# Optimization experiments

Measured on AMD Instinct MI355X. Metric: run time of the kernel, lower is better.

## Reference

```python
import jax, jax.numpy as jnp
import numpy as np

B, MAX_NODE, MEM_LEN, DIM, HEADS, LAYERS, DEG = 32, 1024, 256, 128, 4, 4, 16
CH = DIM // HEADS


def setup_inputs() -> dict:
    key = jax.random.key(0)
    ks = jax.random.split(key, 16)
    counts = np.array([512 + 16 * i for i in range(B)])  # ragged graph sizes, sum = 24320
    N = int(counts.sum())
    node2batch = np.repeat(np.arange(B), counts)
    node2pos = np.concatenate([np.arange(c) for c in counts])
    bmask = np.arange(MAX_NODE)[None, :] < counts[:, None]
    rng = np.random.default_rng(0)
    srcs, dsts, off = [], [], 0
    for c in counts:  # edges stay within each graph
        srcs.append(off + rng.integers(0, c, size=DEG * c))
        dsts.append(off + rng.integers(0, c, size=DEG * c))
        off += c
    edge_index = np.stack([np.concatenate(srcs), np.concatenate(dsts)])

    def rn(k, shape, scale=0.05):
        return jax.random.normal(k, shape, jnp.float32) * scale

    return dict(
        node_feats=rn(ks[0], (N, DIM), 1.0),
        edge_feats=rn(ks[1], (edge_index.shape[1], DIM), 1.0),
        memory=rn(ks[2], (B, MEM_LEN, DIM), 1.0),
        Wn=rn(ks[3], (LAYERS, DIM, DIM)), bn=jnp.zeros((LAYERS, DIM)),
        We=rn(ks[4], (LAYERS, DIM, DIM)),
        att_src=rn(ks[5], (LAYERS, HEADS, CH)),
        att_dst=rn(ks[6], (LAYERS, HEADS, CH)),
        att_edge=rn(ks[7], (LAYERS, HEADS, CH)),
        ln1_g=jnp.ones((LAYERS, DIM)), ln1_b=jnp.zeros((LAYERS, DIM)),
        ln2_g=jnp.ones((LAYERS, DIM)), ln2_b=jnp.zeros((LAYERS, DIM)),
        Wq=rn(ks[8], (LAYERS, DIM, DIM)), Wk=rn(ks[9], (LAYERS, DIM, DIM)),
        Wv=rn(ks[10], (LAYERS, DIM, DIM)), Wo=rn(ks[11], (LAYERS, DIM, DIM)),
        Ew1=rn(ks[12], (LAYERS, 3 * DIM, DIM)), Eb1=jnp.zeros((LAYERS, DIM)),
        Ew2=rn(ks[13], (LAYERS, DIM, DIM)), Eb2=jnp.zeros((LAYERS, DIM)),
        edge_index=jnp.asarray(edge_index, jnp.int32),
        node2batch=jnp.asarray(node2batch, jnp.int32),
        node2pos=jnp.asarray(node2pos, jnp.int32),
        batch_mask=jnp.asarray(bmask),
        mem_pad_mask=jnp.ones((B, MEM_LEN), bool),
    )


def _ln(x, g, b):
    mu = x.mean(-1, keepdims=True)
    v = ((x - mu) ** 2).mean(-1, keepdims=True)
    return (x - mu) * jax.lax.rsqrt(v + 1e-5) * g + b


def reference(node_feats, edge_feats, memory, Wn, bn, We, att_src, att_dst, att_edge,
              ln1_g, ln1_b, ln2_g, ln2_b, Wq, Wk, Wv, Wo, Ew1, Eb1, Ew2, Eb2,
              edge_index, node2batch, node2pos, batch_mask, mem_pad_mask):
    N = node_feats.shape[0]
    src, dst = edge_index[0], edge_index[1]
    # [B, max_node, mem_len]: attend only valid memory slots from valid nodes
    cross_mask = mem_pad_mask[:, None, :] & batch_mask[:, :, None]
    x, e = node_feats, edge_feats
    for l in range(LAYERS):
        # --- edge-conditioned GAT conv (segment softmax over dst) ---
        h = (x @ Wn[l]).reshape(N, HEADS, CH)
        eh = (e @ We[l]).reshape(-1, HEADS, CH)
        logits = (h[src] * att_src[l]).sum(-1) + (h[dst] * att_dst[l]).sum(-1) + (eh * att_edge[l]).sum(-1)
        logits = jax.nn.leaky_relu(logits, 0.2)  # [E, H]
        m = jax.ops.segment_max(logits, dst, num_segments=N)
        ew = jnp.exp(logits - m[dst])
        den = jax.ops.segment_sum(ew, dst, num_segments=N)
        alpha = ew / (den[dst] + 1e-16)
        conv = jax.ops.segment_sum(alpha[..., None] * (h[src] + eh), dst, num_segments=N)
        conv = conv.reshape(N, DIM) + bn[l]
        x = jax.nn.relu(_ln(conv, ln1_g[l], ln1_b[l])) + x
        # --- graph2batch scatter into dense padded tensor ---
        dense = jnp.zeros((B, MAX_NODE, DIM), x.dtype).at[node2batch, node2pos].set(x)
        # --- cross attention against memory ---
        q = (dense @ Wq[l]).reshape(B, MAX_NODE, HEADS, CH)
        k = (memory @ Wk[l]).reshape(B, MEM_LEN, HEADS, CH)
        v = (memory @ Wv[l]).reshape(B, MEM_LEN, HEADS, CH)
        scores = jnp.einsum('bqhc,bkhc->bhqk', q, k) / np.float32(np.sqrt(CH))
        scores = jnp.where(cross_mask[:, None], scores, jnp.float32(-1e9))
        ao = jnp.einsum('bhqk,bkhc->bqhc', jax.nn.softmax(scores, axis=-1), v)
        ao = ao.reshape(B, MAX_NODE, DIM) @ Wo[l]
        dense = jax.nn.relu(_ln(ao + dense, ln2_g[l], ln2_b[l]))
        x = dense[node2batch, node2pos]  # batch2graph gather
        # --- residual sparse edge update ---
        ecat = jnp.concatenate([e, x[src], x[dst]], axis=-1)
        e = e + jax.nn.relu(ecat @ Ew1[l] + Eb1[l]) @ Ew2[l] + Eb2[l]
    return x, e
```

## Files before the change

kernel.cpp:

```cpp
#include <hip/hip_runtime.h>

#define DIM    128
#define HEADS  4
#define CH     32
#define MEMLEN 256
#define LAYERS 4


__global__ void copy_f4(const float4* __restrict__ in, float4* __restrict__ out, long n) {
    long i = (long)blockIdx.x * blockDim.x + threadIdx.x;
    long stride = (long)gridDim.x * blockDim.x;
    for (; i < n; i += stride) out[i] = in[i];
}

__global__ void hist_k(const int* __restrict__ dst, int E, int* __restrict__ deg) {
    int e = blockIdx.x * blockDim.x + threadIdx.x;
    if (e < E) atomicAdd(&deg[dst[e]], 1);
}

__global__ void csr_offsets(const int* __restrict__ deg, int n, int* __restrict__ off) {
    __shared__ int part[1024];
    int t = threadIdx.x;
    int chunk = (n + 1023) >> 10;
    int lo = t * chunk, hi = min(lo + chunk, n);
    int s = 0;
    for (int i = lo; i < hi; i++) s += deg[i];
    part[t] = s; __syncthreads();
    for (int d = 1; d < 1024; d <<= 1) {
        int v = part[t];
        int add = (t >= d) ? part[t - d] : 0;
        __syncthreads();
        part[t] = v + add;
        __syncthreads();
    }
    int run = (t == 0) ? 0 : part[t - 1];
    for (int i = lo; i < hi; i++) { off[i] = run; run += deg[i]; }
    if (t == 1023) off[n] = part[1023];
}

__global__ void csr_fill(const int* __restrict__ dst, int E, const int* __restrict__ off,
                         int* __restrict__ cur, int* __restrict__ csr) {
    int e = blockIdx.x * blockDim.x + threadIdx.x;
    if (e < E) {
        int d = dst[e];
        int p = atomicAdd(&cur[d], 1);
        csr[off[d] + p] = e;
    }
}

__device__ __forceinline__ float block_reduce_sum128(float v, float* red) {
    int t = threadIdx.x;
    red[t] = v; __syncthreads();
#pragma unroll
    for (int s = 64; s > 0; s >>= 1) {
        if (t < s) red[t] += red[t + s];
        __syncthreads();
    }
    float r = red[0]; __syncthreads();
    return r;
}

__global__ __launch_bounds__(256) void gemm128(const float* __restrict__ A,
                                               const float* __restrict__ W,
                                               const float* __restrict__ bias,
                                               float* __restrict__ out, int R) {
    int r0 = blockIdx.x * 64, t = threadIdx.x;
    __shared__ float at[64][DIM];
    for (int i = t; i < 64 * 32; i += 256) {
        int rr = i >> 5, cc = i & 31;
        if (r0 + rr < R)
            ((float4*)at[rr])[cc] = ((const float4*)(A + (size_t)(r0 + rr) * DIM))[cc];
    }
    __syncthreads();
    int c0 = (t & 31) * 4;
    int rb = (t >> 5) * 8;
    float acc[8][4];
#pragma unroll
    for (int ee = 0; ee < 8; ee++)
        acc[ee][0] = acc[ee][1] = acc[ee][2] = acc[ee][3] = 0.f;
    for (int k = 0; k < DIM; k += 4) {
        float4 w0 = *(const float4*)&W[(k + 0) * DIM + c0];
        float4 w1 = *(const float4*)&W[(k + 1) * DIM + c0];
        float4 w2 = *(const float4*)&W[(k + 2) * DIM + c0];
        float4 w3 = *(const float4*)&W[(k + 3) * DIM + c0];
#pragma unroll
        for (int ee = 0; ee < 8; ee++) {
            float4 a = *(float4*)&at[rb + ee][k];
            acc[ee][0] += a.x * w0.x + a.y * w1.x + a.z * w2.x + a.w * w3.x;
            acc[ee][1] += a.x * w0.y + a.y * w1.y + a.z * w2.y + a.w * w3.y;
            acc[ee][2] += a.x * w0.z + a.y * w1.z + a.z * w2.z + a.w * w3.z;
            acc[ee][3] += a.x * w0.w + a.y * w1.w + a.z * w2.w + a.w * w3.w;
        }
    }
    float4 bb = make_float4(0.f, 0.f, 0.f, 0.f);
    if (bias) bb = *(const float4*)&bias[c0];
#pragma unroll
    for (int ee = 0; ee < 8; ee++) {
        int r = r0 + rb + ee;
        if (r < R) {
            float4 o = make_float4(acc[ee][0] + bb.x, acc[ee][1] + bb.y,
                                   acc[ee][2] + bb.z, acc[ee][3] + bb.w);
            *(float4*)&out[(size_t)r * DIM + c0] = o;
        }
    }
}

__global__ __launch_bounds__(256) void node_proj_tile(
    const float* __restrict__ x, const float* __restrict__ W,
    const float* __restrict__ att_s, const float* __restrict__ att_d,
    float* __restrict__ h, float* __restrict__ ssrc, float* __restrict__ sdst, int N) {
    int r0 = blockIdx.x * 64, t = threadIdx.x;
    __shared__ float at[64][DIM];
    for (int i = t; i < 64 * 32; i += 256) {
        int rr = i >> 5, cc = i & 31;
        if (r0 + rr < N)
            ((float4*)at[rr])[cc] = ((const float4*)(x + (size_t)(r0 + rr) * DIM))[cc];
    }
    __syncthreads();
    int c0 = (t & 31) * 4;
    int rb = (t >> 5) * 8;
    float acc[8][4];
#pragma unroll
    for (int ee = 0; ee < 8; ee++)
        acc[ee][0] = acc[ee][1] = acc[ee][2] = acc[ee][3] = 0.f;
    for (int k = 0; k < DIM; k += 4) {
        float4 w0 = *(const float4*)&W[(k + 0) * DIM + c0];
        float4 w1 = *(const float4*)&W[(k + 1) * DIM + c0];
        float4 w2 = *(const float4*)&W[(k + 2) * DIM + c0];
        float4 w3 = *(const float4*)&W[(k + 3) * DIM + c0];
#pragma unroll
        for (int ee = 0; ee < 8; ee++) {
            float4 a = *(float4*)&at[rb + ee][k];
            acc[ee][0] += a.x * w0.x + a.y * w1.x + a.z * w2.x + a.w * w3.x;
            acc[ee][1] += a.x * w0.y + a.y * w1.y + a.z * w2.y + a.w * w3.y;
            acc[ee][2] += a.x * w0.z + a.y * w1.z + a.z * w2.z + a.w * w3.z;
            acc[ee][3] += a.x * w0.w + a.y * w1.w + a.z * w2.w + a.w * w3.w;
        }
    }
    int hh = (t & 31) >> 3;
    float4 as = *(const float4*)&att_s[c0];
    float4 ad = *(const float4*)&att_d[c0];
#pragma unroll
    for (int ee = 0; ee < 8; ee++) {
        int r = r0 + rb + ee;
        if (r < N) {
            *(float4*)&h[(size_t)r * DIM + c0] =
                make_float4(acc[ee][0], acc[ee][1], acc[ee][2], acc[ee][3]);
            float ps = acc[ee][0]*as.x + acc[ee][1]*as.y + acc[ee][2]*as.z + acc[ee][3]*as.w;
            float pd = acc[ee][0]*ad.x + acc[ee][1]*ad.y + acc[ee][2]*ad.z + acc[ee][3]*ad.w;
#pragma unroll
            for (int mk = 1; mk < 8; mk <<= 1) {
                ps += __shfl_xor(ps, mk, 32);
                pd += __shfl_xor(pd, mk, 32);
            }
            if (((t & 31) & 7) == 0) {
                ssrc[r * HEADS + hh] = ps;
                sdst[r * HEADS + hh] = pd;
            }
        }
    }
}


__global__ void make_waE(const float* __restrict__ We, const float* __restrict__ att_e,
                         float* __restrict__ waE) {
    int k = threadIdx.x;
#pragma unroll
    for (int h = 0; h < HEADS; h++) {
        float s = 0.f;
#pragma unroll
        for (int c = 0; c < CH; c++) s += We[k * DIM + h * CH + c] * att_e[h * CH + c];
        waE[k * HEADS + h] = s;
    }
}

__global__ void sedge_logits(const float* __restrict__ e, const float* __restrict__ waE,
                             const float* __restrict__ ssrc, const float* __restrict__ sdst,
                             const int* __restrict__ src, const int* __restrict__ dst,
                             float* __restrict__ lw, int E) {
    __shared__ float w[DIM * HEADS];
    int t = threadIdx.x;
    w[t] = waE[t]; w[t + 256] = waE[t + 256];
    __syncthreads();
    int g = t >> 5, lane = t & 31;
    int eid = blockIdx.x * 8 + g;
    if (eid >= E) return;
    const float* er = e + (size_t)eid * DIM;
    float s0 = 0.f, s1 = 0.f, s2 = 0.f, s3 = 0.f;
#pragma unroll
    for (int j = 0; j < 4; j++) {
        int k = lane + 32 * j;
        float v = er[k];
        s0 += v * w[k * 4 + 0]; s1 += v * w[k * 4 + 1];
        s2 += v * w[k * 4 + 2]; s3 += v * w[k * 4 + 3];
    }
#pragma unroll
    for (int m = 16; m; m >>= 1) {
        s0 += __shfl_xor(s0, m, 32); s1 += __shfl_xor(s1, m, 32);
        s2 += __shfl_xor(s2, m, 32); s3 += __shfl_xor(s3, m, 32);
    }
    if (lane == 0) {
        int sn = src[eid] * HEADS, dn = dst[eid] * HEADS;
        float l0 = ssrc[sn + 0] + sdst[dn + 0] + s0;
        float l1 = ssrc[sn + 1] + sdst[dn + 1] + s1;
        float l2 = ssrc[sn + 2] + sdst[dn + 2] + s2;
        float l3 = ssrc[sn + 3] + sdst[dn + 3] + s3;
        lw[eid * 4 + 0] = (l0 >= 0.f) ? l0 : 0.2f * l0;
        lw[eid * 4 + 1] = (l1 >= 0.f) ? l1 : 0.2f * l1;
        lw[eid * 4 + 2] = (l2 >= 0.f) ? l2 : 0.2f * l2;
        lw[eid * 4 + 3] = (l3 >= 0.f) ? l3 : 0.2f * l3;
    }
}

__global__ void seg_softmax(const int* __restrict__ off, const int* __restrict__ csr,
                            float* __restrict__ lw, float* __restrict__ den, int NH) {
    int i = blockIdx.x * blockDim.x + threadIdx.x;
    if (i >= NH) return;
    int n = i >> 2, hh = i & 3;
    int o0 = off[n], o1 = off[n + 1];
    float m = -1e30f;
    for (int o = o0; o < o1; o++) m = fmaxf(m, lw[csr[o] * HEADS + hh]);
    float s = 0.f;
    for (int o = o0; o < o1; o++) {
        int idx = csr[o] * HEADS + hh;
        float w = __expf(lw[idx] - m);
        lw[idx] = w;
        s += w;
    }
    den[i] = s;
}

__global__ void conv_ln(const int* __restrict__ off, const int* __restrict__ csr,
                        const int* __restrict__ src,
                        const float* __restrict__ lw, const float* __restrict__ den,
                        const float* __restrict__ hbuf, const float* __restrict__ e,
                        const float* __restrict__ We,
                        const float* __restrict__ bn, const float* __restrict__ g,
                        const float* __restrict__ b, float* __restrict__ x, int N) {
    int n = blockIdx.x, t = threadIdx.x, hh = t >> 5;
    __shared__ float agge[HEADS][DIM];
    __shared__ float red[DIM];
    int o0 = off[n], o1 = off[n + 1];
    float acch = 0.f, a0 = 0.f, a1 = 0.f, a2 = 0.f, a3 = 0.f;
    for (int o = o0; o < o1; o++) {
        int eid = csr[o];
        int s = src[eid];
        float4 al = *(const float4*)&lw[eid * 4];
        acch += ((&al.x)[hh]) * hbuf[(size_t)s * DIM + t];
        float ev = e[(size_t)eid * DIM + t];
        a0 += al.x * ev; a1 += al.y * ev; a2 += al.z * ev; a3 += al.w * ev;
    }
    agge[0][t] = a0; agge[1][t] = a1; agge[2][t] = a2; agge[3][t] = a3;
    __syncthreads();
    float ehc = 0.f;
#pragma unroll 8
    for (int k = 0; k < DIM; k++) ehc += agge[hh][k] * We[k * DIM + t];
    float d = den[n * HEADS + hh];
    float conv = (acch + ehc) / (d + 1e-16f) + bn[t];
    float mu = block_reduce_sum128(conv, red) * (1.f / DIM);
    float diff = conv - mu;
    float var = block_reduce_sum128(diff * diff, red) * (1.f / DIM);
    float y = diff * rsqrtf(var + 1e-5f) * g[t] + b[t];
    x[(size_t)n * DIM + t] = fmaxf(y, 0.f) + x[(size_t)n * DIM + t];
}

__global__ void kv_proj(const float* __restrict__ mem, const float* __restrict__ Wk,
                        const float* __restrict__ Wv, float* __restrict__ kb,
                        float* __restrict__ vb, int R) {
    int r = blockIdx.x, t = threadIdx.x;
    __shared__ float row[DIM];
    row[t] = mem[(size_t)r * DIM + t];
    __syncthreads();
    float ak = 0.f, av = 0.f;
#pragma unroll 4
    for (int k = 0; k < DIM; k++) {
        float rv = row[k];
        ak += rv * Wk[k * DIM + t];
        av += rv * Wv[k * DIM + t];
    }
    kb[(size_t)r * DIM + t] = ak;
    vb[(size_t)r * DIM + t] = av;
}

__global__ __launch_bounds__(256) void cross_attn_tile(
    float* __restrict__ x, const float* __restrict__ qg,
    const float* __restrict__ kb, const float* __restrict__ vb,
    const float* __restrict__ Wo, const float* __restrict__ g,
    const float* __restrict__ b, const int* __restrict__ boff) {
    int bb = blockIdx.y;
    int n0 = boff[bb] + blockIdx.x * 64;
    int cnt = boff[bb + 1] - n0;
    if (cnt <= 0) return;
    int nq = min(64, cnt);
    int t = threadIdx.x;
    int q = t & 63, h = t >> 6;

    __shared__ float smem[64 * 132];

    float qv[32];
    if (q < nq) {
        const float4* qp = (const float4*)(qg + (size_t)(n0 + q) * DIM + h * CH);
#pragma unroll
        for (int j = 0; j < 8; j++) {
            float4 v = qp[j];
            qv[4*j+0] = v.x; qv[4*j+1] = v.y; qv[4*j+2] = v.z; qv[4*j+3] = v.w;
        }
    } else {
#pragma unroll
        for (int c = 0; c < 32; c++) qv[c] = 0.f;
    }

    float oacc[32];
#pragma unroll
    for (int c = 0; c < 32; c++) oacc[c] = 0.f;
    float m = -1e30f, l = 0.f;

    const float4* Ksrc = (const float4*)(kb + (size_t)bb * MEMLEN * DIM);
    const float4* Vsrc = (const float4*)(vb + (size_t)bb * MEMLEN * DIM);
    float4* Kl = (float4*)smem;
    float4* Vl = (float4*)(smem + 32 * DIM);

    for (int ch = 0; ch < MEMLEN / 32; ch++) {
        __syncthreads();
#pragma unroll
        for (int r = 0; r < 4; r++) {
            int idx = t + r * 256;
            Kl[idx] = Ksrc[ch * 1024 + idx];
            Vl[idx] = Vsrc[ch * 1024 + idx];
        }
        __syncthreads();
        float sc[32];
#pragma unroll
        for (int kk = 0; kk < 32; kk++) {
            const float* kp = smem + kk * DIM + h * CH;
            float s = 0.f;
#pragma unroll
            for (int c = 0; c < 32; c++) s += qv[c] * kp[c];
            sc[kk] = s * 0.17677669529663689f;
        }
        float mc = sc[0];
#pragma unroll
        for (int kk = 1; kk < 32; kk++) mc = fmaxf(mc, sc[kk]);
        float mn = fmaxf(m, mc);
        float scale = __expf(m - mn);
        m = mn;
        float ls = 0.f;
#pragma unroll
        for (int kk = 0; kk < 32; kk++) {
            float w = __expf(sc[kk] - mn);
            sc[kk] = w;
            ls += w;
        }
        l = l * scale + ls;
#pragma unroll
        for (int c = 0; c < 32; c++) oacc[c] *= scale;
#pragma unroll
        for (int kk = 0; kk < 32; kk++) {
            const float* vp = smem + 32 * DIM + kk * DIM + h * CH;
            float w = sc[kk];
#pragma unroll
            for (int c = 0; c < 32; c++) oacc[c] += w * vp[c];
        }
    }
    __syncthreads();
    {
        float inv = 1.f / l;
        float* ap = smem + q * 132 + h * CH;
#pragma unroll
        for (int c = 0; c < 32; c++) ap[c] = oacc[c] * inv;
    }
    __syncthreads();
    int c0 = (t & 31) * 4;
    int rb = (t >> 5) * 8;
    float acc2[8][4];
#pragma unroll
    for (int ee = 0; ee < 8; ee++)
        acc2[ee][0] = acc2[ee][1] = acc2[ee][2] = acc2[ee][3] = 0.f;
    for (int k = 0; k < DIM; k += 4) {
        float4 w0 = *(const float4*)&Wo[(k + 0) * DIM + c0];
        float4 w1 = *(const float4*)&Wo[(k + 1) * DIM + c0];
        float4 w2 = *(const float4*)&Wo[(k + 2) * DIM + c0];
        float4 w3 = *(const float4*)&Wo[(k + 3) * DIM + c0];
#pragma unroll
        for (int ee = 0; ee < 8; ee++) {
            float4 a = *(const float4*)(smem + (rb + ee) * 132 + k);
            acc2[ee][0] += a.x * w0.x + a.y * w1.x + a.z * w2.x + a.w * w3.x;
            acc2[ee][1] += a.x * w0.y + a.y * w1.y + a.z * w2.y + a.w * w3.y;
            acc2[ee][2] += a.x * w0.z + a.y * w1.z + a.z * w2.z + a.w * w3.z;
            acc2[ee][3] += a.x * w0.w + a.y * w1.w + a.z * w2.w + a.w * w3.w;
        }
    }
    float4 gg = *(const float4*)&g[c0];
    float4 bb4 = *(const float4*)&b[c0];
#pragma unroll
    for (int ee = 0; ee < 8; ee++) {
        int r = rb + ee;
        if (r < nq) {
            float4 xr = *(const float4*)&x[(size_t)(n0 + r) * DIM + c0];
            float o0 = acc2[ee][0] + xr.x, o1 = acc2[ee][1] + xr.y;
            float o2 = acc2[ee][2] + xr.z, o3 = acc2[ee][3] + xr.w;
            float s1 = o0 + o1 + o2 + o3;
#pragma unroll
            for (int mk = 16; mk; mk >>= 1) s1 += __shfl_xor(s1, mk, 32);
            float mu = s1 * (1.f / DIM);
            float d0 = o0 - mu, d1 = o1 - mu, d2 = o2 - mu, d3 = o3 - mu;
            float s2 = d0*d0 + d1*d1 + d2*d2 + d3*d3;
#pragma unroll
            for (int mk = 16; mk; mk >>= 1) s2 += __shfl_xor(s2, mk, 32);
            float rs = rsqrtf(s2 * (1.f / DIM) + 1e-5f);
            float4 o = make_float4(fmaxf(d0 * rs * gg.x + bb4.x, 0.f),
                                   fmaxf(d1 * rs * gg.y + bb4.y, 0.f),
                                   fmaxf(d2 * rs * gg.z + bb4.z, 0.f),
                                   fmaxf(d3 * rs * gg.w + bb4.w, 0.f));
            *(float4*)&x[(size_t)(n0 + r) * DIM + c0] = o;
        }
    }
}

__global__ __launch_bounds__(256) void edge_mlp(float* __restrict__ e,
                                                const float* __restrict__ xs,
                                                const float* __restrict__ xd,
                                                const int* __restrict__ src,
                                                const int* __restrict__ dst,
                                                const float* __restrict__ W1,
                                                const float* __restrict__ W2,
                                                const float* __restrict__ Eb2, int E) {
    int e0 = blockIdx.x * 64, t = threadIdx.x;
    __shared__ float at[64][DIM];
    for (int i = t; i < 64 * 32; i += 256) {
        int rr = i >> 5, cc = i & 31;
        if (e0 + rr < E)
            ((float4*)at[rr])[cc] = ((const float4*)(e + (size_t)(e0 + rr) * DIM))[cc];
    }
    __syncthreads();
    int c0 = (t & 31) * 4;
    int rb = (t >> 5) * 8;
    float acc[8][4];
#pragma unroll
    for (int ee = 0; ee < 8; ee++)
        acc[ee][0] = acc[ee][1] = acc[ee][2] = acc[ee][3] = 0.f;
    for (int k = 0; k < DIM; k += 4) {
        float4 w0 = *(const float4*)&W1[(k + 0) * DIM + c0];
        float4 w1 = *(const float4*)&W1[(k + 1) * DIM + c0];
        float4 w2 = *(const float4*)&W1[(k + 2) * DIM + c0];
        float4 w3 = *(const float4*)&W1[(k + 3) * DIM + c0];
#pragma unroll
        for (int ee = 0; ee < 8; ee++) {
            float4 a = *(float4*)&at[rb + ee][k];
            acc[ee][0] += a.x * w0.x + a.y * w1.x + a.z * w2.x + a.w * w3.x;
            acc[ee][1] += a.x * w0.y + a.y * w1.y + a.z * w2.y + a.w * w3.y;
            acc[ee][2] += a.x * w0.z + a.y * w1.z + a.z * w2.z + a.w * w3.z;
            acc[ee][3] += a.x * w0.w + a.y * w1.w + a.z * w2.w + a.w * w3.w;
        }
    }
#pragma unroll
    for (int ee = 0; ee < 8; ee++) {
        int r = e0 + rb + ee;
        if (r < E) {
            float4 s4 = *(const float4*)&xs[(size_t)src[r] * DIM + c0];
            float4 d4 = *(const float4*)&xd[(size_t)dst[r] * DIM + c0];
            acc[ee][0] = fmaxf(acc[ee][0] + s4.x + d4.x, 0.f);
            acc[ee][1] = fmaxf(acc[ee][1] + s4.y + d4.y, 0.f);
            acc[ee][2] = fmaxf(acc[ee][2] + s4.z + d4.z, 0.f);
            acc[ee][3] = fmaxf(acc[ee][3] + s4.w + d4.w, 0.f);
        }
    }
    __syncthreads();
#pragma unroll
    for (int ee = 0; ee < 8; ee++)
        *(float4*)&at[rb + ee][c0] = make_float4(acc[ee][0], acc[ee][1], acc[ee][2], acc[ee][3]);
    __syncthreads();
#pragma unroll
    for (int ee = 0; ee < 8; ee++)
        acc[ee][0] = acc[ee][1] = acc[ee][2] = acc[ee][3] = 0.f;
    for (int k = 0; k < DIM; k += 4) {
        float4 w0 = *(const float4*)&W2[(k + 0) * DIM + c0];
        float4 w1 = *(const float4*)&W2[(k + 1) * DIM + c0];
        float4 w2 = *(const float4*)&W2[(k + 2) * DIM + c0];
        float4 w3 = *(const float4*)&W2[(k + 3) * DIM + c0];
#pragma unroll
        for (int ee = 0; ee < 8; ee++) {
            float4 a = *(float4*)&at[rb + ee][k];
            acc[ee][0] += a.x * w0.x + a.y * w1.x + a.z * w2.x + a.w * w3.x;
            acc[ee][1] += a.x * w0.y + a.y * w1.y + a.z * w2.y + a.w * w3.y;
            acc[ee][2] += a.x * w0.z + a.y * w1.z + a.z * w2.z + a.w * w3.z;
            acc[ee][3] += a.x * w0.w + a.y * w1.w + a.z * w2.w + a.w * w3.w;
        }
    }
    float4 b2 = *(const float4*)&Eb2[c0];
#pragma unroll
    for (int ee = 0; ee < 8; ee++) {
        int r = e0 + rb + ee;
        if (r < E) {
            float4 old = *(const float4*)&e[(size_t)r * DIM + c0];
            float4 o = make_float4(old.x + acc[ee][0] + b2.x, old.y + acc[ee][1] + b2.y,
                                   old.z + acc[ee][2] + b2.z, old.w + acc[ee][3] + b2.w);
            *(float4*)&e[(size_t)r * DIM + c0] = o;
        }
    }
}


extern "C" void kernel_launch(void* const* d_in, const int* in_sizes, int n_in,
                              void* d_out, int out_size, void* d_ws, size_t ws_size,
                              hipStream_t stream) {
    const float* node_feats = (const float*)d_in[0];
    const float* edge_feats = (const float*)d_in[1];
    const float* memory     = (const float*)d_in[2];
    const float* Wn   = (const float*)d_in[3];
    const float* bn   = (const float*)d_in[4];
    const float* We   = (const float*)d_in[5];
    const float* att_src  = (const float*)d_in[6];
    const float* att_dst  = (const float*)d_in[7];
    const float* att_edge = (const float*)d_in[8];
    const float* ln1_g = (const float*)d_in[9];
    const float* ln1_b = (const float*)d_in[10];
    const float* ln2_g = (const float*)d_in[11];
    const float* ln2_b = (const float*)d_in[12];
    const float* Wq = (const float*)d_in[13];
    const float* Wk = (const float*)d_in[14];
    const float* Wv = (const float*)d_in[15];
    const float* Wo = (const float*)d_in[16];
    const float* Ew1 = (const float*)d_in[17];
    const float* Eb1 = (const float*)d_in[18];
    const float* Ew2 = (const float*)d_in[19];
    const float* Eb2 = (const float*)d_in[20];
    const int* edge_index = (const int*)d_in[21];
    const int* node2batch = (const int*)d_in[22];

    const int N = in_sizes[0] / DIM;
    const int E = in_sizes[1] / DIM;
    const int Bn = in_sizes[2] / (MEMLEN * DIM);
    const int* srcA = edge_index;
    const int* dstA = edge_index + E;

    float* x = (float*)d_out;
    float* e = x + (size_t)N * DIM;

    char* p = (char*)d_ws;
    auto carve = [&](size_t bytes) {
        void* r = (void*)p;
        p += (bytes + 255) & ~(size_t)255;
        return r;
    };
    float* h     = (float*)carve((size_t)N * DIM * 4);
    float* qg    = (float*)carve((size_t)N * DIM * 4);
    float* xs    = (float*)carve((size_t)N * DIM * 4);
    float* xd    = (float*)carve((size_t)N * DIM * 4);
    float* ssrc  = (float*)carve((size_t)N * HEADS * 4);
    float* sdst  = (float*)carve((size_t)N * HEADS * 4);
    float* lw    = (float*)carve((size_t)E * HEADS * 4);
    float* den   = (float*)carve((size_t)N * HEADS * 4);
    float* waE   = (float*)carve((size_t)DIM * HEADS * 4);
    float* kbuf  = (float*)carve((size_t)Bn * MEMLEN * DIM * 4);
    float* vbuf  = (float*)carve((size_t)Bn * MEMLEN * DIM * 4);
    int* deg     = (int*)carve((size_t)N * 4);
    int* cur     = (int*)carve((size_t)N * 4);
    int* off     = (int*)carve(((size_t)N + 1) * 4);
    int* csr     = (int*)carve((size_t)E * 4);
    int* bcnt    = (int*)carve((size_t)Bn * 4);
    int* boff    = (int*)carve(((size_t)Bn + 1) * 4);

    {
        long nx = (long)N * DIM / 4;
        copy_f4<<<dim3(2048), dim3(256), 0, stream>>>((const float4*)node_feats, (float4*)x, nx);
        long nen = (long)E * DIM / 4;
        copy_f4<<<dim3(4096), dim3(256), 0, stream>>>((const float4*)edge_feats, (float4*)e, nen);
    }

    hipMemsetAsync(deg, 0, (size_t)N * 4, stream);
    hipMemsetAsync(cur, 0, (size_t)N * 4, stream);
    hipMemsetAsync(bcnt, 0, (size_t)Bn * 4, stream);
    hist_k<<<dim3((E + 255) / 256), dim3(256), 0, stream>>>(dstA, E, deg);
    csr_offsets<<<dim3(1), dim3(1024), 0, stream>>>(deg, N, off);
    csr_fill<<<dim3((E + 255) / 256), dim3(256), 0, stream>>>(dstA, E, off, cur, csr);
    hist_k<<<dim3((N + 255) / 256), dim3(256), 0, stream>>>(node2batch, N, bcnt);
    csr_offsets<<<dim3(1), dim3(1024), 0, stream>>>(bcnt, Bn, boff);

    const int mrows = Bn * MEMLEN;
    const int maxTiles = 1024 / 64;
    for (int l = 0; l < LAYERS; l++) {
        const float* Wn_l  = Wn  + (size_t)l * DIM * DIM;
        const float* We_l  = We  + (size_t)l * DIM * DIM;
        const float* Wq_l  = Wq  + (size_t)l * DIM * DIM;
        const float* Wk_l  = Wk  + (size_t)l * DIM * DIM;
        const float* Wv_l  = Wv  + (size_t)l * DIM * DIM;
        const float* Wo_l  = Wo  + (size_t)l * DIM * DIM;
        const float* Ew1_l = Ew1 + (size_t)l * 3 * DIM * DIM;
        const float* Ew2_l = Ew2 + (size_t)l * DIM * DIM;

        node_proj_tile<<<dim3((N + 63) / 64), dim3(256), 0, stream>>>(
            x, Wn_l, att_src + l * DIM, att_dst + l * DIM, h, ssrc, sdst, N);
        make_waE<<<dim3(1), dim3(DIM), 0, stream>>>(We_l, att_edge + l * DIM, waE);
        sedge_logits<<<dim3((E + 7) / 8), dim3(256), 0, stream>>>(
            e, waE, ssrc, sdst, srcA, dstA, lw, E);
        seg_softmax<<<dim3((N * HEADS + 255) / 256), dim3(256), 0, stream>>>(
            off, csr, lw, den, N * HEADS);
        conv_ln<<<dim3(N), dim3(DIM), 0, stream>>>(
            off, csr, srcA, lw, den, h, e, We_l,
            bn + l * DIM, ln1_g + l * DIM, ln1_b + l * DIM, x, N);
        kv_proj<<<dim3(mrows), dim3(DIM), 0, stream>>>(
            memory, Wk_l, Wv_l, kbuf, vbuf, mrows);
        gemm128<<<dim3((N + 63) / 64), dim3(256), 0, stream>>>(
            x, Wq_l, nullptr, qg, N);
        cross_attn_tile<<<dim3(maxTiles, Bn), dim3(256), 0, stream>>>(
            x, qg, kbuf, vbuf, Wo_l, ln2_g + l * DIM, ln2_b + l * DIM, boff);
        gemm128<<<dim3((N + 63) / 64), dim3(256), 0, stream>>>(
            x, Ew1_l + (size_t)DIM * DIM, Eb1 + l * DIM, xs, N);
        gemm128<<<dim3((N + 63) / 64), dim3(256), 0, stream>>>(
            x, Ew1_l + (size_t)2 * DIM * DIM, nullptr, xd, N);
        edge_mlp<<<dim3((E + 63) / 64), dim3(256), 0, stream>>>(
            e, xs, xd, srcA, dstA, Ew1_l, Ew2_l, Eb2 + l * DIM, E);
    }
}
```

Baseline: 4.300 ms.

## Split conv aggregation across four edge partitions, retile edge MLP, use gemm for KV

Replaces the per-node 128-thread conv_ln with a 512-thread variant that divides each node's incoming edges over four partitions, reduces the partial sums in shared memory, and uses wave shuffles for the layernorm reductions. The edge MLP is retiled to 4 rows by 8 columns per thread with padded shared rows. The per-row kv_proj kernel is replaced by two calls to the tiled gemm128. The aim is more parallelism per node and better register reuse in the edge GEMMs, at the cost of extra shared-memory reductions and one more launch.

Measured after the change: 4.336 ms. Within noise of the previous version (+0.8%).

```diff
diff --git a/kernel.cpp b/kernel.cpp
--- a/kernel.cpp
+++ b/kernel.cpp
@@ -48,18 +48,6 @@
     }
 }
 
-__device__ __forceinline__ float block_reduce_sum128(float v, float* red) {
-    int t = threadIdx.x;
-    red[t] = v; __syncthreads();
-#pragma unroll
-    for (int s = 64; s > 0; s >>= 1) {
-        if (t < s) red[t] += red[t + s];
-        __syncthreads();
-    }
-    float r = red[0]; __syncthreads();
-    return r;
-}
-
 __global__ __launch_bounds__(256) void gemm128(const float* __restrict__ A,
                                                const float* __restrict__ W,
                                                const float* __restrict__ bias,
@@ -230,56 +218,63 @@
     den[i] = s;
 }
 
-__global__ void conv_ln(const int* __restrict__ off, const int* __restrict__ csr,
-                        const int* __restrict__ src,
-                        const float* __restrict__ lw, const float* __restrict__ den,
-                        const float* __restrict__ hbuf, const float* __restrict__ e,
-                        const float* __restrict__ We,
-                        const float* __restrict__ bn, const float* __restrict__ g,
-                        const float* __restrict__ b, float* __restrict__ x, int N) {
-    int n = blockIdx.x, t = threadIdx.x, hh = t >> 5;
-    __shared__ float agge[HEADS][DIM];
-    __shared__ float red[DIM];
+__global__ __launch_bounds__(512) void conv_ln4(
+    const int* __restrict__ off, const int* __restrict__ csr, const int* __restrict__ src,
+    const float* __restrict__ lw, const float* __restrict__ den,
+    const float* __restrict__ hbuf, const float* __restrict__ e, const float* __restrict__ We,
+    const float* __restrict__ bn, const float* __restrict__ g, const float* __restrict__ b,
+    float* __restrict__ x, int N) {
+    int t = threadIdx.x;
+    int tt = t & 127, part = t >> 7;
+    int n = blockIdx.x;
+    int hh = tt >> 5;
+    __shared__ float aggeP[4][HEADS][DIM];
+    __shared__ float acchP[4][DIM];
+    __shared__ float ehcP[4][DIM];
+    __shared__ float wred[16];
     int o0 = off[n], o1 = off[n + 1];
     float acch = 0.f, a0 = 0.f, a1 = 0.f, a2 = 0.f, a3 = 0.f;
-    for (int o = o0; o < o1; o++) {
+    for (int o = o0 + part; o < o1; o += 4) {
         int eid = csr[o];
         int s = src[eid];
         float4 al = *(const float4*)&lw[eid * 4];
-        acch += ((&al.x)[hh]) * hbuf[(size_t)s * DIM + t];
-        float ev = e[(size_t)eid * DIM + t];
+        acch += ((&al.x)[hh]) * hbuf[(size_t)s * DIM + tt];
+        float ev = e[(size_t)eid * DIM + tt];
         a0 += al.x * ev; a1 += al.y * ev; a2 += al.z * ev; a3 += al.w * ev;
     }
-    agge[0][t] = a0; agge[1][t] = a1; agge[2][t] = a2; agge[3][t] = a3;
+    aggeP[part][0][tt] = a0; aggeP[part][1][tt] = a1;
+    aggeP[part][2][tt] = a2; aggeP[part][3][tt] = a3;
+    acchP[part][tt] = acch;
     __syncthreads();
     float ehc = 0.f;
-#pragma unroll 8
-    for (int k = 0; k < DIM; k++) ehc += agge[hh][k] * We[k * DIM + t];
-    float d = den[n * HEADS + hh];
-    float conv = (acch + ehc) / (d + 1e-16f) + bn[t];
-    float mu = block_reduce_sum128(conv, red) * (1.f / DIM);
+    int k0 = part * 32;
+    for (int k = k0; k < k0 + 32; k++) {
+        float ag = aggeP[0][hh][k] + aggeP[1][hh][k] + aggeP[2][hh][k] + aggeP[3][hh][k];
+        ehc += ag * We[k * DIM + tt];
+    }
+    ehcP[part][tt] = ehc;
+    __syncthreads();
+    float conv = (acchP[0][tt] + acchP[1][tt] + acchP[2][tt] + acchP[3][tt]
+                + ehcP[0][tt] + ehcP[1][tt] + ehcP[2][tt] + ehcP[3][tt])
+                 / (den[n * HEADS + hh] + 1e-16f) + bn[tt];
+    int w = t >> 6;
+    float s1 = conv;
+#pragma unroll
+    for (int mk = 32; mk; mk >>= 1) s1 += __shfl_xor(s1, mk, 64);
+    if ((t & 63) == 0) wred[w] = s1;
+    __syncthreads();
+    float mu = (wred[w] + wred[w ^ 1]) * (1.f / DIM);
     float diff = conv - mu;
-    float var = block_reduce_sum128(diff * diff, red) * (1.f / DIM);
-    float y = diff * rsqrtf(var + 1e-5f) * g[t] + b[t];
-    x[(size_t)n * DIM + t] = fmaxf(y, 0.f) + x[(size_t)n * DIM + t];
-}
-
-__global__ void kv_proj(const float* __restrict__ mem, const float* __restrict__ Wk,
-                        const float* __restrict__ Wv, float* __restrict__ kb,
-                        float* __restrict__ vb, int R) {
-    int r = blockIdx.x, t = threadIdx.x;
-    __shared__ float row[DIM];
-    row[t] = mem[(size_t)r * DIM + t];
-    __syncthreads();
-    float ak = 0.f, av = 0.f;
-#pragma unroll 4
-    for (int k = 0; k < DIM; k++) {
-        float rv = row[k];
-        ak += rv * Wk[k * DIM + t];
-        av += rv * Wv[k * DIM + t];
-    }
-    kb[(size_t)r * DIM + t] = ak;
-    vb[(size_t)r * DIM + t] = av;
+    float s2 = diff * diff;
+#pragma unroll
+    for (int mk = 32; mk; mk >>= 1) s2 += __shfl_xor(s2, mk, 64);
+    if ((t & 63) == 0) wred[8 + w] = s2;
+    __syncthreads();
+    float var = (wred[8 + w] + wred[8 + (w ^ 1)]) * (1.f / DIM);
+    if (part == 0) {
+        float y = diff * rsqrtf(var + 1e-5f) * g[tt] + b[tt];
+        x[(size_t)n * DIM + tt] = fmaxf(y, 0.f) + x[(size_t)n * DIM + tt];
+    }
 }
 
 __global__ __launch_bounds__(256) void cross_attn_tile(
@@ -417,85 +412,119 @@
     }
 }
 
-__global__ __launch_bounds__(256) void edge_mlp(float* __restrict__ e,
-                                                const float* __restrict__ xs,
-                                                const float* __restrict__ xd,
-                                                const int* __restrict__ src,
-                                                const int* __restrict__ dst,
-                                                const float* __restrict__ W1,
-                                                const float* __restrict__ W2,
-                                                const float* __restrict__ Eb2, int E) {
+__global__ __launch_bounds__(256, 4) void edge_mlp(float* __restrict__ e,
+                                                   const float* __restrict__ xs,
+                                                   const float* __restrict__ xd,
+                                                   const int* __restrict__ src,
+                                                   const int* __restrict__ dst,
+                                                   const float* __restrict__ W1,
+                                                   const float* __restrict__ W2,
+                                                   const float* __restrict__ Eb2, int E) {
     int e0 = blockIdx.x * 64, t = threadIdx.x;
-    __shared__ float at[64][DIM];
+    int tx = t & 15, ty = t >> 4;
+    int c0 = tx * 8;
+    __shared__ float at[64][130];
     for (int i = t; i < 64 * 32; i += 256) {
         int rr = i >> 5, cc = i & 31;
         if (e0 + rr < E)
-            ((float4*)at[rr])[cc] = ((const float4*)(e + (size_t)(e0 + rr) * DIM))[cc];
-    }
-    __syncthreads();
-    int c0 = (t & 31) * 4;
-    int rb = (t >> 5) * 8;
-    float acc[8][4];
-#pragma unroll
-    for (int ee = 0; ee < 8; ee++)
-        acc[ee][0] = acc[ee][1] = acc[ee][2] = acc[ee][3] = 0.f;
+            *(float4*)&at[rr][cc * 4] = *(const float4*)&e[(size_t)(e0 + rr) * DIM + cc * 4];
+    }
+    __syncthreads();
+    float acc[4][8];
+#pragma unroll
+    for (int r = 0; r < 4; r++)
+#pragma unroll
+        for (int c = 0; c < 8; c++) acc[r][c] = 0.f;
     for (int k = 0; k < DIM; k += 4) {
-        float4 w0 = *(const float4*)&W1[(k + 0) * DIM + c0];
-        float4 w1 = *(const float4*)&W1[(k + 1) * DIM + c0];
-        float4 w2 = *(const float4*)&W1[(k + 2) * DIM + c0];
-        float4 w3 = *(const float4*)&W1[(k + 3) * DIM + c0];
-#pragma unroll
-        for (int ee = 0; ee < 8; ee++) {
-            float4 a = *(float4*)&at[rb + ee][k];
-            acc[ee][0] += a.x * w0.x + a.y * w1.x + a.z * w2.x + a.w * w3.x;
-            acc[ee][1] += a.x * w0.y + a.y * w1.y + a.z * w2.y + a.w * w3.y;
-            acc[ee][2] += a.x * w0.z + a.y * w1.z + a.z * w2.z + a.w * w3.z;
-            acc[ee][3] += a.x * w0.w + a.y * w1.w + a.z * w2.w + a.w * w3.w;
-        }
-    }
-#pragma unroll
-    for (int ee = 0; ee < 8; ee++) {
-        int r = e0 + rb + ee;
-        if (r < E) {
-            float4 s4 = *(const float4*)&xs[(size_t)src[r] * DIM + c0];
-            float4 d4 = *(const float4*)&xd[(size_t)dst[r] * DIM + c0];
-            acc[ee][0] = fmaxf(acc[ee][0] + s4.x + d4.x, 0.f);
-            acc[ee][1] = fmaxf(acc[ee][1] + s4.y + d4.y, 0.f);
-            acc[ee][2] = fmaxf(acc[ee][2] + s4.z + d4.z, 0.f);
-            acc[ee][3] = fmaxf(acc[ee][3] + s4.w + d4.w, 0.f);
-        }
-    }
-    __syncthreads();
-#pragma unroll
-    for (int ee = 0; ee < 8; ee++)
-        *(float4*)&at[rb + ee][c0] = make_float4(acc[ee][0], acc[ee][1], acc[ee][2], acc[ee][3]);
-    __syncthreads();
-#pragma unroll
-    for (int ee = 0; ee < 8; ee++)
-        acc[ee][0] = acc[ee][1] = acc[ee][2] = acc[ee][3] = 0.f;
+        float4 a4[4];
+#pragma unroll
+        for (int r = 0; r < 4; r++) a4[r] = *(const float4*)&at[ty * 4 + r][k];
+        float4 wv[8];
+#pragma unroll
+        for (int kk = 0; kk < 4; kk++) {
+            wv[2*kk]   = *(const float4*)&W1[(size_t)(k + kk) * DIM + c0];
+            wv[2*kk+1] = *(const float4*)&W1[(size_t)(k + kk) * DIM + c0 + 4];
+        }
+#pragma unroll
+        for (int kk = 0; kk < 4; kk++) {
+#pragma unroll
+            for (int r = 0; r < 4; r++) {
+                float av = (&a4[r].x)[kk];
+                float4 w0 = wv[2*kk], w1 = wv[2*kk+1];
+                acc[r][0] += av * w0.x; acc[r][1] += av * w0.y;
+                acc[r][2] += av * w0.z; acc[r][3] += av * w0.w;
+                acc[r][4] += av * w1.x; acc[r][5] += av * w1.y;
+                acc[r][6] += av * w1.z; acc[r][7] += av * w1.w;
+            }
+        }
+    }
+#pragma unroll
+    for (int r = 0; r < 4; r++) {
+        int row = e0 + ty * 4 + r;
+        if (row < E) {
+            int sr = src[row], dr = dst[row];
+            float4 s0 = *(const float4*)&xs[(size_t)sr * DIM + c0];
+            float4 s1 = *(const float4*)&xs[(size_t)sr * DIM + c0 + 4];
+            float4 d0 = *(const float4*)&xd[(size_t)dr * DIM + c0];
+            float4 d1 = *(const float4*)&xd[(size_t)dr * DIM + c0 + 4];
+            acc[r][0] = fmaxf(acc[r][0] + s0.x + d0.x, 0.f);
+            acc[r][1] = fmaxf(acc[r][1] + s0.y + d0.y, 0.f);
+            acc[r][2] = fmaxf(acc[r][2] + s0.z + d0.z, 0.f);
+            acc[r][3] = fmaxf(acc[r][3] + s0.w + d0.w, 0.f);
+            acc[r][4] = fmaxf(acc[r][4] + s1.x + d1.x, 0.f);
+            acc[r][5] = fmaxf(acc[r][5] + s1.y + d1.y, 0.f);
+            acc[r][6] = fmaxf(acc[r][6] + s1.z + d1.z, 0.f);
+            acc[r][7] = fmaxf(acc[r][7] + s1.w + d1.w, 0.f);
+        }
+    }
+    __syncthreads();
+#pragma unroll
+    for (int r = 0; r < 4; r++) {
+        *(float4*)&at[ty * 4 + r][c0]     = make_float4(acc[r][0], acc[r][1], acc[r][2], acc[r][3]);
+        *(float4*)&at[ty * 4 + r][c0 + 4] = make_float4(acc[r][4], acc[r][5], acc[r][6], acc[r][7]);
+    }
+    __syncthreads();
+#pragma unroll
+    for (int r = 0; r < 4; r++)
+#pragma unroll
+        for (int c = 0; c < 8; c++) acc[r][c] = 0.f;
     for (int k = 0; k < DIM; k += 4) {
-        float4 w0 = *(const float4*)&W2[(k + 0) * DIM + c0];
-        float4 w1 = *(const float4*)&W2[(k + 1) * DIM + c0];
-        float4 w2 = *(const float4*)&W2[(k + 2) * DIM + c0];
-        float4 w3 = *(const float4*)&W2[(k + 3) * DIM + c0];
-#pragma unroll
-        for (int ee = 0; ee < 8; ee++) {
-            float4 a = *(float4*)&at[rb + ee][k];
-            acc[ee][0] += a.x * w0.x + a.y * w1.x + a.z * w2.x + a.w * w3.x;
-            acc[ee][1] += a.x * w0.y + a.y * w1.y + a.z * w2.y + a.w * w3.y;
-            acc[ee][2] += a.x * w0.z + a.y * w1.z + a.z * w2.z + a.w * w3.z;
-            acc[ee][3] += a.x * w0.w + a.y * w1.w + a.z * w2.w + a.w * w3.w;
-        }
-    }
-    float4 b2 = *(const float4*)&Eb2[c0];
-#pragma unroll
-    for (int ee = 0; ee < 8; ee++) {
-        int r = e0 + rb + ee;
-        if (r < E) {
-            float4 old = *(const float4*)&e[(size_t)r * DIM + c0];
-            float4 o = make_float4(old.x + acc[ee][0] + b2.x, old.y + acc[ee][1] + b2.y,
-                                   old.z + acc[ee][2] + b2.z, old.w + acc[ee][3] + b2.w);
-            *(float4*)&e[(size_t)r * DIM + c0] = o;
+        float4 a4[4];
+#pragma unroll
+        for (int r = 0; r < 4; r++) a4[r] = *(const float4*)&at[ty * 4 + r][k];
+        float4 wv[8];
+#pragma unroll
+        for (int kk = 0; kk < 4; kk++) {
+            wv[2*kk]   = *(const float4*)&W2[(size_t)(k + kk) * DIM + c0];
+            wv[2*kk+1] = *(const float4*)&W2[(size_t)(k + kk) * DIM + c0 + 4];
+        }
+#pragma unroll
+        for (int kk = 0; kk < 4; kk++) {
+#pragma unroll
+            for (int r = 0; r < 4; r++) {
+                float av = (&a4[r].x)[kk];
+                float4 w0 = wv[2*kk], w1 = wv[2*kk+1];
+                acc[r][0] += av * w0.x; acc[r][1] += av * w0.y;
+                acc[r][2] += av * w0.z; acc[r][3] += av * w0.w;
+                acc[r][4] += av * w1.x; acc[r][5] += av * w1.y;
+                acc[r][6] += av * w1.z; acc[r][7] += av * w1.w;
+            }
+        }
+    }
+    float4 b20 = *(const float4*)&Eb2[c0];
+    float4 b21 = *(const float4*)&Eb2[c0 + 4];
+#pragma unroll
+    for (int r = 0; r < 4; r++) {
+        int row = e0 + ty * 4 + r;
+        if (row < E) {
+            float4 o0 = *(const float4*)&e[(size_t)row * DIM + c0];
+            float4 o1 = *(const float4*)&e[(size_t)row * DIM + c0 + 4];
+            o0.x += acc[r][0] + b20.x; o0.y += acc[r][1] + b20.y;
+            o0.z += acc[r][2] + b20.z; o0.w += acc[r][3] + b20.w;
+            o1.x += acc[r][4] + b21.x; o1.y += acc[r][5] + b21.y;
+            o1.z += acc[r][6] + b21.z; o1.w += acc[r][7] + b21.w;
+            *(float4*)&e[(size_t)row * DIM + c0]     = o0;
+            *(float4*)&e[(size_t)row * DIM + c0 + 4] = o1;
         }
     }
 }
@@ -596,11 +625,13 @@
             e, waE, ssrc, sdst, srcA, dstA, lw, E);
         seg_softmax<<<dim3((N * HEADS + 255) / 256), dim3(256), 0, stream>>>(
             off, csr, lw, den, N * HEADS);
-        conv_ln<<<dim3(N), dim3(DIM), 0, stream>>>(
+        conv_ln4<<<dim3(N), dim3(512), 0, stream>>>(
             off, csr, srcA, lw, den, h, e, We_l,
             bn + l * DIM, ln1_g + l * DIM, ln1_b + l * DIM, x, N);
-        kv_proj<<<dim3(mrows), dim3(DIM), 0, stream>>>(
-            memory, Wk_l, Wv_l, kbuf, vbuf, mrows);
+        gemm128<<<dim3((mrows + 63) / 64), dim3(256), 0, stream>>>(
+            memory, Wk_l, nullptr, kbuf, mrows);
+        gemm128<<<dim3((mrows + 63) / 64), dim3(256), 0, stream>>>(
+            memory, Wv_l, nullptr, vbuf, mrows);
         gemm128<<<dim3((N + 63) / 64), dim3(256), 0, stream>>>(
             x, Wq_l, nullptr, qg, N);
         cross_attn_tile<<<dim3(maxTiles, Bn), dim3(256), 0, stream>>>(
```
